# Optimization experiments

Hardware: AMD Instinct MI355X
Metric: run time of the kernel (lower is better)

The kernel has to match this reference:

```python
import jax, jax.numpy as jnp
import numpy as np

B, S, H, V = 32, 400, 512, 50000


def setup_inputs() -> dict:
    key = jax.random.key(0)
    ks = jax.random.split(key, 32)
    g = lambda i, shape: jax.random.normal(ks[i], shape, jnp.float32) * 0.05
    return {
        "x_id": jax.random.randint(ks[0], (B, S), 0, V, jnp.int32),
        "y_id": jax.random.randint(ks[1], (B, 1), 0, V, jnp.int32),
        "x_mask": jnp.zeros((B, S), jnp.int32),  # pad flag: 1 = pad
        "emb": g(2, (V, H)),
        "enc_fw_W": g(3, (H, 3 * H)), "enc_fw_U": g(4, (H, 3 * H)), "enc_fw_b": g(5, (2, 3 * H)),
        "enc_bw_W": g(6, (H, 3 * H)), "enc_bw_U": g(7, (H, 3 * H)), "enc_bw_b": g(8, (2, 3 * H)),
        "red_W": g(9, (2 * H, H)), "red_b": g(10, (H,)),
        "dec_W": g(11, (H, 3 * H)), "dec_U": g(12, (H, 3 * H)), "dec_b": g(13, (2, 3 * H)),
        "att_Wh": g(14, (2 * H, H)), "att_Ws": g(15, (H, H)), "att_bs": g(16, (H,)),
        "att_Wc": g(17, (1, 1)), "att_V": g(18, (H, 1)),
        "fc_W": g(19, (3 * H, H)), "fc_b": g(20, (H,)),
        "vocab_W": g(21, (H, V)),
        "pg_Wh": g(22, (2 * H, 1)), "pg_Ws": g(23, (H, 1)), "pg_Wx": g(24, (H, 1)), "pg_b": g(25, (1,)),
    }


def _gru_cell(h, xz, U, br):
    # Keras GRU, reset_after=True, gate order z, r, h
    hd = h.shape[-1]
    rec = h @ U + br
    z = jax.nn.sigmoid(xz[..., :hd] + rec[..., :hd])
    r = jax.nn.sigmoid(xz[..., hd:2 * hd] + rec[..., hd:2 * hd])
    hh = jnp.tanh(xz[..., 2 * hd:] + r * rec[..., 2 * hd:])
    return z * h + (1.0 - z) * hh


def _gru_scan(x, h0, W, U, b):
    xz = x @ W + b[0]  # [b,T,3H] -- input projections precomputed
    def step(h, xt):
        h = _gru_cell(h, xt, U, b[1])
        return h, h
    h_last, hs = jax.lax.scan(step, h0, jnp.swapaxes(xz, 0, 1))
    return jnp.swapaxes(hs, 0, 1), h_last


def reference(x_id, y_id, x_mask, emb, enc_fw_W, enc_fw_U, enc_fw_b, enc_bw_W, enc_bw_U, enc_bw_b,
              red_W, red_b, dec_W, dec_U, dec_b, att_Wh, att_Ws, att_bs, att_Wc, att_V,
              fc_W, fc_b, vocab_W, pg_Wh, pg_Ws, pg_Wx, pg_b):
    b, s = x_id.shape
    hid = enc_fw_U.shape[0]
    maskf = x_mask.astype(jnp.float32)
    # ---- encoder: single-layer BiGRU ----
    x_emb = emb[x_id]                                     # [b,S,H]
    h0 = jnp.zeros((b, hid), x_emb.dtype)
    fw_seq, fw_s = _gru_scan(x_emb, h0, enc_fw_W, enc_fw_U, enc_fw_b)
    bw_seq, bw_s = _gru_scan(x_emb[:, ::-1], h0, enc_bw_W, enc_bw_U, enc_bw_b)
    enc_seq = jnp.concatenate([fw_seq, bw_seq[:, ::-1]], -1)   # [b,S,2H]
    state = jax.nn.relu(jnp.concatenate([fw_s, bw_s], -1) @ red_W + red_b)  # [b,H]
    # ---- decoder: one GRU step ----
    y_emb = emb[y_id]                                     # [b,1,H]
    xz = y_emb[:, 0] @ dec_W + dec_b[0]
    dec_state = _gru_cell(state, xz, dec_U, dec_b[1])     # [b,H]
    dec_out = dec_state[:, None, :]                       # [b,1,H]
    # ---- Bahdanau attention with (zero-initialized) coverage ----
    e = enc_seq @ att_Wh + (dec_out @ att_Ws + att_bs)    # [b,S,H]
    cover = jnp.zeros((b, s, 1), e.dtype)
    e = e + cover @ att_Wc
    e = jnp.tanh(e) @ att_V                               # [b,S,1]
    e = e + maskf[..., None] * -1e10
    w = jax.nn.softmax(e, axis=-2)                        # [b,S,1]
    context = jnp.sum(w * enc_seq, axis=-2, keepdims=True)  # [b,1,2H]
    # ---- output projection + vocab softmax ----
    y_out = jnp.concatenate([dec_out, context], -1) @ fc_W + fc_b  # [b,1,H]
    vocab_dist = jax.nn.softmax(y_out[:, 0] @ vocab_W, axis=-1)    # [b,V]
    # ---- pointer gate ----
    p_gen = jax.nn.sigmoid(context[:, 0] @ pg_Wh + dec_state @ pg_Ws + y_emb[:, 0] @ pg_Wx + pg_b)  # [b,1]
    # ---- extended-vocab copy distribution (vectorized batched scatter-add) ----
    aw = w[..., 0] * (1.0 - maskf) * (1.0 - p_gen)        # [b,S]
    ext = jnp.pad(p_gen * vocab_dist, ((0, 0), (0, s)))   # [b,V+S]
    bidx = jnp.arange(b)[:, None]
    final = ext.at[bidx, x_id].add(aw)                    # [b,V+S]
    return final
```

## Files before the change

### kernel.cpp

```cpp
#include <hip/hip_runtime.h>
#include <math.h>

#define S_LEN 400
#define BATCH 32
#define HID   512
#define G3    1536
#define N2    3072
#define VOC   50000
#define OUTW  (VOC + S_LEN)

typedef unsigned long long ull;
typedef unsigned int uint;
typedef unsigned short ushort;
typedef short bf16x8 __attribute__((ext_vector_type(8)));
typedef float f32x4 __attribute__((ext_vector_type(4)));
typedef ushort u16x8 __attribute__((ext_vector_type(8)));

__device__ __forceinline__ float sigf(float x) { return 1.f / (1.f + __expf(-x)); }
__device__ __forceinline__ float tanh_fast(float x) {
  const float xc = fminf(fmaxf(x, -15.f), 15.f);
  const float e = __expf(-2.f * xc);
  return (1.f - e) / (1.f + e);
}
__device__ __forceinline__ ushort f2bf(float f) {
  uint u = __float_as_uint(f);
  u += 0x7FFFu + ((u >> 16) & 1u);
  return (ushort)(u >> 16);
}
__device__ __forceinline__ float bf2f(ushort h) {
  return __uint_as_float((uint)h << 16);
}
__device__ __forceinline__ float dot4(float4 a, float4 b) {
  return a.x*b.x + a.y*b.y + a.z*b.z + a.w*b.w;
}

__global__ __launch_bounds__(512) void gru_scan(
    const ushort* __restrict__ xzm,
    const ushort* __restrict__ Utbf,
    const float* __restrict__ bfw, const float* __restrict__ bbw,
    float* __restrict__ enc_seq, ushort* __restrict__ enc_bf,
    ull* __restrict__ hpkt)
{
  const int bid = blockIdx.x;
  const int group = bid & 7;
  const int dir = group >> 2;
  const int bg  = group & 3;
  const int ht  = bid >> 3;
  const int tid = threadIdx.x;
  const int lane = tid & 63;
  const int w  = tid >> 6;
  const int l15 = lane & 15;
  const int lk  = lane >> 4;

  const float* __restrict__ br = (dir ? bbw : bfw) + G3;

  const int gate = w % 3, jh = w / 3;
  bf16x8 ufrag[16];
  if (w < 6) {
    const ushort* ub = Utbf + ((size_t)dir * G3 + gate * 512 + ht * 32 + jh * 16 + l15) * 512
                     + lk * 8;
    #pragma unroll
    for (int s = 0; s < 16; ++s)
      ufrag[s] = *(const bf16x8*)(ub + s * 32);
  }

  __shared__ ushort h_bf[16][520];
  __shared__ float redm[3][8][32];

  for (int i = tid; i < 16 * 520; i += 512) ((ushort*)h_bf)[i] = 0;

  const int cb = w;
  const int gbi = tid >> 5;
  const int gj  = tid & 31;
  const int gjq = ht * 32 + gj;
  const int gb  = bg * 8 + (gbi & 7);
  const float brz = br[gjq], brr = br[512 + gjq], brh = br[1024 + gjq];

  ull* __restrict__ pk = hpkt + (size_t)dir * (2 * BATCH * HID);
  __syncthreads();

  for (int t = 0; t < S_LEN; ++t) {
    const int ts = dir ? (S_LEN - 1 - t) : t;

    float xzv0 = 0.f, xzv1 = 0.f, xzv2 = 0.f;
    if (tid < 256) {
      const ushort* xp = xzm + ((size_t)gb * S_LEN + ts) * N2 + dir * G3 + gjq;
      xzv0 = bf2f(xp[0]); xzv1 = bf2f(xp[512]); xzv2 = bf2f(xp[1024]);
    }

    float hold = 0.f;
    {
      ull* bp = pk + ((size_t)(t & 1) * BATCH + (bg * 8 + cb)) * HID + lane;
      ull* hp = pk + ((size_t)(t & 1) * BATCH + gb) * HID + gjq;
      const uint tu = (uint)t;
      for (;;) {
        ull v0 = __hip_atomic_load(bp,       __ATOMIC_RELAXED, __HIP_MEMORY_SCOPE_AGENT);
        ull v1 = __hip_atomic_load(bp + 64,  __ATOMIC_RELAXED, __HIP_MEMORY_SCOPE_AGENT);
        ull v2 = __hip_atomic_load(bp + 128, __ATOMIC_RELAXED, __HIP_MEMORY_SCOPE_AGENT);
        ull v3 = __hip_atomic_load(bp + 192, __ATOMIC_RELAXED, __HIP_MEMORY_SCOPE_AGENT);
        ull v4 = __hip_atomic_load(bp + 256, __ATOMIC_RELAXED, __HIP_MEMORY_SCOPE_AGENT);
        ull v5 = __hip_atomic_load(bp + 320, __ATOMIC_RELAXED, __HIP_MEMORY_SCOPE_AGENT);
        ull v6 = __hip_atomic_load(bp + 384, __ATOMIC_RELAXED, __HIP_MEMORY_SCOPE_AGENT);
        ull v7 = __hip_atomic_load(bp + 448, __ATOMIC_RELAXED, __HIP_MEMORY_SCOPE_AGENT);
        bool ok = ((uint)(v0 >> 32) == tu) & ((uint)(v1 >> 32) == tu)
                & ((uint)(v2 >> 32) == tu) & ((uint)(v3 >> 32) == tu)
                & ((uint)(v4 >> 32) == tu) & ((uint)(v5 >> 32) == tu)
                & ((uint)(v6 >> 32) == tu) & ((uint)(v7 >> 32) == tu);
        ull hv = 0;
        if (tid < 256) {
          hv = __hip_atomic_load(hp, __ATOMIC_RELAXED, __HIP_MEMORY_SCOPE_AGENT);
          ok &= ((uint)(hv >> 32) == tu);
        }
        if (__all(ok)) {
          h_bf[cb][lane]       = f2bf(__uint_as_float((uint)v0));
          h_bf[cb][lane + 64]  = f2bf(__uint_as_float((uint)v1));
          h_bf[cb][lane + 128] = f2bf(__uint_as_float((uint)v2));
          h_bf[cb][lane + 192] = f2bf(__uint_as_float((uint)v3));
          h_bf[cb][lane + 256] = f2bf(__uint_as_float((uint)v4));
          h_bf[cb][lane + 320] = f2bf(__uint_as_float((uint)v5));
          h_bf[cb][lane + 384] = f2bf(__uint_as_float((uint)v6));
          h_bf[cb][lane + 448] = f2bf(__uint_as_float((uint)v7));
          if (tid < 256) hold = __uint_as_float((uint)hv);
          break;
        }
        __builtin_amdgcn_s_sleep(1);
      }
    }
    __syncthreads();

    if (w < 6) {
      f32x4 acc = f32x4{0.f, 0.f, 0.f, 0.f};
      #pragma unroll
      for (int s = 0; s < 16; ++s) {
        const bf16x8 af = *(const bf16x8*)&h_bf[l15][s * 32 + lk * 8];
        acc = __builtin_amdgcn_mfma_f32_16x16x32_bf16(af, ufrag[s], acc, 0, 0, 0);
      }
      if (lk < 2) {
        #pragma unroll
        for (int r = 0; r < 4; ++r)
          redm[gate][lk * 4 + r][jh * 16 + l15] = acc[r];
      }
    }
    __syncthreads();

    if (tid < 256) {
      const float rz = redm[0][gbi][gj] + brz;
      const float rr = redm[1][gbi][gj] + brr;
      const float rh = redm[2][gbi][gj] + brh;
      const float z  = sigf(xzv0 + rz);
      const float r  = sigf(xzv1 + rr);
      const float hh = tanh_fast(xzv2 + r * rh);
      const float hnew = z * hold + (1.f - z) * hh;
      const ull pack = ((ull)(uint)(t + 1) << 32) | (ull)__float_as_uint(hnew);
      __hip_atomic_store(pk + ((size_t)((t + 1) & 1) * BATCH + gb) * HID + gjq,
                         pack, __ATOMIC_RELAXED, __HIP_MEMORY_SCOPE_AGENT);
      const size_t eidx = ((size_t)gb * S_LEN + ts) * 1024 + dir * 512 + gjq;
      enc_seq[eidx] = hnew;
      enc_bf[eidx]  = f2bf(hnew);
    }
    __syncthreads();
  }
}

__global__ __launch_bounds__(256) void k_transW(
    const float* __restrict__ srcA, const float* __restrict__ srcB,
    const int split, const int srcStride, const int Krows,
    ushort* __restrict__ dst,
    const float* __restrict__ biasA, const float* __restrict__ biasB,
    float* __restrict__ bm)
{
  __shared__ float t[64][65];
  const int k0 = blockIdx.x * 64, n0 = blockIdx.y * 64;
  const int tid = threadIdx.x;
  const int j = tid & 63, i0 = tid >> 6;
  {
    const int n = n0 + j;
    const float* s = (n < split) ? (srcA + n) : (srcB + (n - split));
    #pragma unroll
    for (int i = i0; i < 64; i += 4)
      t[i][j] = s[(size_t)(k0 + i) * srcStride];
  }
  __syncthreads();
  const int ii = tid & 63;
  #pragma unroll
  for (int jj = i0; jj < 64; jj += 4)
    dst[(size_t)(n0 + jj) * Krows + k0 + ii] = f2bf(t[ii][jj]);
  if (bm != nullptr && k0 == 0 && tid < 64) {
    const int n = n0 + tid;
    bm[n] = (n < split) ? biasA[n] : biasB[n - split];
  }
}

__global__ __launch_bounds__(256) void k_transF(
    const float* __restrict__ srcA, const float* __restrict__ srcB,
    const int split, const int srcStride, const int Krows,
    float* __restrict__ dst)
{
  __shared__ float t[64][65];
  const int k0 = blockIdx.x * 64, n0 = blockIdx.y * 64;
  const int tid = threadIdx.x;
  const int j = tid & 63, i0 = tid >> 6;
  {
    const int n = n0 + j;
    const float* s = (n < split) ? (srcA + n) : (srcB + (n - split));
    #pragma unroll
    for (int i = i0; i < 64; i += 4)
      t[i][j] = s[(size_t)(k0 + i) * srcStride];
  }
  __syncthreads();
  const int ii = tid & 63;
  #pragma unroll
  for (int jj = i0; jj < 64; jj += 4)
    dst[(size_t)(n0 + jj) * Krows + k0 + ii] = t[ii][jj];
}

__global__ __launch_bounds__(256) void gemm_bf16(
    const int* __restrict__ x_id, const float* __restrict__ emb,
    const ushort* __restrict__ Bt,
    const float* __restrict__ bias,
    ushort* __restrict__ C)
{
  const int m0 = blockIdx.y * 128, n0 = blockIdx.x * 128;
  const int tid = threadIdx.x;
  const int w = tid >> 6, lane = tid & 63;
  const int l15 = lane & 15, lk = lane >> 4;
  __shared__ short As[128][40];
  __shared__ short Bs[128][40];
  __shared__ int rid[128];
  if (tid < 128) rid[tid] = x_id[m0 + tid];
  f32x4 acc[2][8];
  #pragma unroll
  for (int i = 0; i < 2; ++i)
    #pragma unroll
    for (int j = 0; j < 8; ++j) acc[i][j] = f32x4{0.f, 0.f, 0.f, 0.f};

  const int sr = tid >> 1;
  const int sc = (tid & 1) * 8;
  __syncthreads();
  const float* arow = emb + (size_t)rid[sr] * 512;

  for (int k0 = 0; k0 < 512; k0 += 32) {
    const float4 f0 = *(const float4*)(arow + k0 + sc);
    const float4 f1 = *(const float4*)(arow + k0 + sc + 4);
    const float4 f2 = *(const float4*)(arow + k0 + 16 + sc);
    const float4 f3 = *(const float4*)(arow + k0 + 16 + sc + 4);
    const uint4 b0 = *(const uint4*)&Bt[(size_t)(n0 + sr) * 512 + k0 + sc];
    const uint4 b1 = *(const uint4*)&Bt[(size_t)(n0 + sr) * 512 + k0 + 16 + sc];
    u16x8 a0, a1;
    a0[0]=f2bf(f0.x); a0[1]=f2bf(f0.y); a0[2]=f2bf(f0.z); a0[3]=f2bf(f0.w);
    a0[4]=f2bf(f1.x); a0[5]=f2bf(f1.y); a0[6]=f2bf(f1.z); a0[7]=f2bf(f1.w);
    a1[0]=f2bf(f2.x); a1[1]=f2bf(f2.y); a1[2]=f2bf(f2.z); a1[3]=f2bf(f2.w);
    a1[4]=f2bf(f3.x); a1[5]=f2bf(f3.y); a1[6]=f2bf(f3.z); a1[7]=f2bf(f3.w);
    *(u16x8*)&As[sr][sc]      = a0;
    *(u16x8*)&As[sr][16 + sc] = a1;
    *(uint4*)&Bs[sr][sc]      = b0;
    *(uint4*)&Bs[sr][16 + sc] = b1;
    __syncthreads();

    bf16x8 af[2], bfr[8];
    #pragma unroll
    for (int rf = 0; rf < 2; ++rf)
      af[rf] = *(const bf16x8*)&As[w * 32 + rf * 16 + l15][lk * 8];
    #pragma unroll
    for (int cf = 0; cf < 8; ++cf)
      bfr[cf] = *(const bf16x8*)&Bs[cf * 16 + l15][lk * 8];
    #pragma unroll
    for (int rf = 0; rf < 2; ++rf)
      #pragma unroll
      for (int cf = 0; cf < 8; ++cf)
        acc[rf][cf] = __builtin_amdgcn_mfma_f32_16x16x32_bf16(
            af[rf], bfr[cf], acc[rf][cf], 0, 0, 0);
    __syncthreads();
  }

  #pragma unroll
  for (int rf = 0; rf < 2; ++rf) {
    #pragma unroll
    for (int cf = 0; cf < 8; ++cf) {
      const int col = n0 + cf * 16 + l15;
      const float bv = bias[col];
      const int rowb = m0 + w * 32 + rf * 16 + lk * 4;
      #pragma unroll
      for (int r = 0; r < 4; ++r)
        C[(size_t)(rowb + r) * N2 + col] = f2bf(acc[rf][cf][r] + bv);
    }
  }
}

__global__ __launch_bounds__(256) void gemm_att(
    const ushort* __restrict__ A,
    const ushort* __restrict__ Bt,
    const float* __restrict__ dterm,
    const float* __restrict__ attV,
    float* __restrict__ e_part)
{
  const int m0 = blockIdx.y * 128, n0 = blockIdx.x * 128;
  const int tid = threadIdx.x;
  const int w = tid >> 6, lane = tid & 63;
  const int l15 = lane & 15, lk = lane >> 4;
  __shared__ short As[128][40];
  __shared__ short Bs[128][40];
  f32x4 acc[2][8];
  #pragma unroll
  for (int i = 0; i < 2; ++i)
    #pragma unroll
    for (int j = 0; j < 8; ++j) acc[i][j] = f32x4{0.f, 0.f, 0.f, 0.f};

  const int sr = tid >> 1;
  const int sc = (tid & 1) * 8;

  for (int k0 = 0; k0 < 1024; k0 += 32) {
    const uint4 a0 = *(const uint4*)&A[(size_t)(m0 + sr) * 1024 + k0 + sc];
    const uint4 a1 = *(const uint4*)&A[(size_t)(m0 + sr) * 1024 + k0 + 16 + sc];
    const uint4 b0 = *(const uint4*)&Bt[(size_t)(n0 + sr) * 1024 + k0 + sc];
    const uint4 b1 = *(const uint4*)&Bt[(size_t)(n0 + sr) * 1024 + k0 + 16 + sc];
    *(uint4*)&As[sr][sc]      = a0;
    *(uint4*)&As[sr][16 + sc] = a1;
    *(uint4*)&Bs[sr][sc]      = b0;
    *(uint4*)&Bs[sr][16 + sc] = b1;
    __syncthreads();

    bf16x8 af[2], bfr[8];
    #pragma unroll
    for (int rf = 0; rf < 2; ++rf)
      af[rf] = *(const bf16x8*)&As[w * 32 + rf * 16 + l15][lk * 8];
    #pragma unroll
    for (int cf = 0; cf < 8; ++cf)
      bfr[cf] = *(const bf16x8*)&Bs[cf * 16 + l15][lk * 8];
    #pragma unroll
    for (int rf = 0; rf < 2; ++rf)
      #pragma unroll
      for (int cf = 0; cf < 8; ++cf)
        acc[rf][cf] = __builtin_amdgcn_mfma_f32_16x16x32_bf16(
            af[rf], bfr[cf], acc[rf][cf], 0, 0, 0);
    __syncthreads();
  }

  #pragma unroll
  for (int rf = 0; rf < 2; ++rf) {
    #pragma unroll
    for (int r = 0; r < 4; ++r) {
      const int row = m0 + w * 32 + rf * 16 + lk * 4 + r;
      const int b = row / S_LEN;
      float p = 0.f;
      #pragma unroll
      for (int cf = 0; cf < 8; ++cf) {
        const int col = n0 + cf * 16 + l15;
        p += attV[col] * tanh_fast(acc[rf][cf][r] + dterm[(size_t)b * 512 + col]);
      }
      p += __shfl_xor(p, 1); p += __shfl_xor(p, 2);
      p += __shfl_xor(p, 4); p += __shfl_xor(p, 8);
      if (l15 == 0) e_part[(size_t)row * 4 + blockIdx.x] = p;
    }
  }
}

__global__ __launch_bounds__(128) void k_state(const float* __restrict__ enc,
    const float* __restrict__ redWt,
    const float* __restrict__ red_b, float* __restrict__ state)
{
  const int b = blockIdx.y;
  const int j = blockIdx.x*128 + threadIdx.x;
  const float4* wr = (const float4*)(redWt + (size_t)j * 1024);
  const float4* fw = (const float4*)(enc + ((size_t)b*S_LEN + (S_LEN-1))*1024);
  const float4* bw = (const float4*)(enc + ((size_t)b*S_LEN)*1024 + 512);
  float acc = red_b[j];
  #pragma unroll 4
  for (int k = 0; k < 128; ++k) acc += dot4(fw[k], wr[k]);
  #pragma unroll 4
  for (int k = 0; k < 128; ++k) acc += dot4(bw[k], wr[128 + k]);
  state[(size_t)b*512 + j] = fmaxf(acc, 0.f);
}

__global__ __launch_bounds__(128) void k_dec(
    const int* __restrict__ y_id, const float* __restrict__ emb,
    const float* __restrict__ state,
    const float* __restrict__ decWUt,
    const float* __restrict__ dec_b, float* __restrict__ dst)
{
  const int b = blockIdx.y;
  const int j = blockIdx.x*128 + threadIdx.x;
  const float4* ye = (const float4*)(emb + (size_t)y_id[b] * 512);
  const float4* st = (const float4*)(state + (size_t)b * 512);
  const float4* w0 = (const float4*)(decWUt + (size_t)(j)        * 512);
  const float4* w1 = (const float4*)(decWUt + (size_t)(512  + j) * 512);
  const float4* w2 = (const float4*)(decWUt + (size_t)(1024 + j) * 512);
  const float4* u0 = (const float4*)(decWUt + (size_t)(G3 + j)        * 512);
  const float4* u1 = (const float4*)(decWUt + (size_t)(G3 + 512  + j) * 512);
  const float4* u2 = (const float4*)(decWUt + (size_t)(G3 + 1024 + j) * 512);
  float xz0 = dec_b[j], xz1 = dec_b[512+j], xz2 = dec_b[1024+j];
  float rc0 = dec_b[G3+j], rc1 = dec_b[G3+512+j], rc2 = dec_b[G3+1024+j];
  #pragma unroll 2
  for (int k = 0; k < 128; ++k) {
    const float4 yv = ye[k], sv = st[k];
    xz0 += dot4(yv, w0[k]); xz1 += dot4(yv, w1[k]); xz2 += dot4(yv, w2[k]);
    rc0 += dot4(sv, u0[k]); rc1 += dot4(sv, u1[k]); rc2 += dot4(sv, u2[k]);
  }
  const float z  = sigf(xz0 + rc0);
  const float r  = sigf(xz1 + rc1);
  const float hh = tanh_fast(xz2 + r*rc2);
  const float sj = state[(size_t)b*512 + j];
  dst[(size_t)b*512 + j] = z*sj + (1.f-z)*hh;
}

__global__ __launch_bounds__(128) void k_dterm(const float* __restrict__ dec,
    const float* __restrict__ WsT,
    const float* __restrict__ att_bs, float* __restrict__ dterm)
{
  const int b = blockIdx.y;
  const int j = blockIdx.x*128 + threadIdx.x;
  const float4* d = (const float4*)(dec + (size_t)b*512);
  const float4* wr = (const float4*)(WsT + (size_t)j * 512);
  float acc = att_bs[j];
  #pragma unroll 4
  for (int k = 0; k < 128; ++k) acc += dot4(d[k], wr[k]);
  dterm[(size_t)b*512 + j] = acc;
}

__global__ __launch_bounds__(512) void k_soft(const float* __restrict__ e_part,
    const int* __restrict__ x_mask, float* __restrict__ wat)
{
  const int b = blockIdx.x, tid = threadIdx.x;
  __shared__ float sm[512];
  float e = -1e30f, ev = 0.f;
  if (tid < S_LEN) {
    const float* ep = e_part + (size_t)(b*S_LEN + tid)*4;
    ev = ep[0]+ep[1]+ep[2]+ep[3] + (float)x_mask[b*S_LEN+tid] * -1e10f;
    e = ev;
  }
  sm[tid] = e; __syncthreads();
  for (int s = 256; s > 0; s >>= 1) { if (tid < s) sm[tid] = fmaxf(sm[tid], sm[tid+s]); __syncthreads(); }
  const float m = sm[0]; __syncthreads();
  const float x = (tid < S_LEN) ? __expf(ev - m) : 0.f;
  sm[tid] = x; __syncthreads();
  for (int s = 256; s > 0; s >>= 1) { if (tid < s) sm[tid] += sm[tid+s]; __syncthreads(); }
  const float inv = 1.f / sm[0];
  if (tid < S_LEN) wat[b*S_LEN+tid] = x * inv;
}

__global__ __launch_bounds__(128) void k_ctx(const float* __restrict__ wat,
    const float* __restrict__ enc, float* __restrict__ ctx)
{
  const int b = blockIdx.y;
  const int j = blockIdx.x*128 + threadIdx.x;
  float acc = 0.f;
  const float* w = wat + b*S_LEN;
  const float* ep = enc + (size_t)b*S_LEN*1024 + j;
  #pragma unroll 4
  for (int s = 0; s < S_LEN; ++s) acc += w[s] * ep[(size_t)s*1024];
  ctx[(size_t)b*1024 + j] = acc;
}

__global__ __launch_bounds__(128) void k_yout(const float* __restrict__ dec,
    const float* __restrict__ ctx,
    const float* __restrict__ fcT,
    const float* __restrict__ fc_b, float* __restrict__ y_out)
{
  const int b = blockIdx.y;
  const int j = blockIdx.x*128 + threadIdx.x;
  const float4* d = (const float4*)(dec + (size_t)b*512);
  const float4* c = (const float4*)(ctx + (size_t)b*1024);
  const float4* wr = (const float4*)(fcT + (size_t)j * 1536);
  float acc = fc_b[j];
  #pragma unroll 4
  for (int k = 0; k < 128; ++k) acc += dot4(d[k], wr[k]);
  #pragma unroll 4
  for (int k = 0; k < 256; ++k) acc += dot4(c[k], wr[128 + k]);
  y_out[(size_t)b*512 + j] = acc;
}

__global__ __launch_bounds__(256) void k_pgen(const float* __restrict__ ctx,
    const float* __restrict__ dec,
    const int* __restrict__ y_id, const float* __restrict__ emb,
    const float* __restrict__ pg_Wh, const float* __restrict__ pg_Ws,
    const float* __restrict__ pg_Wx, const float* __restrict__ pg_b,
    float* __restrict__ pg)
{
  const int b = blockIdx.x, tid = threadIdx.x;
  __shared__ float sm[256];
  const float* ye = emb + (size_t)y_id[b] * 512;
  float acc = 0.f;
  for (int k = tid; k < 1024; k += 256) acc += ctx[(size_t)b*1024+k]*pg_Wh[k];
  for (int k = tid; k < 512;  k += 256) acc += dec[(size_t)b*512+k]*pg_Ws[k] + ye[k]*pg_Wx[k];
  sm[tid] = acc; __syncthreads();
  for (int s = 128; s > 0; s >>= 1) { if (tid < s) sm[tid] += sm[tid+s]; __syncthreads(); }
  if (tid == 0) pg[b] = sigf(sm[0] + pg_b[0]);
}

__global__ __launch_bounds__(256) void k_vocab(const float* __restrict__ y_out,
    const float* __restrict__ vocab_W, float* __restrict__ logits)
{
  __shared__ float y_lds[256][32];
  const int tid = threadIdx.x;
  const int vq = tid & 63, bq = tid >> 6;
  const int v = blockIdx.x * 256 + vq * 4;
  float acc[8][4];
  #pragma unroll
  for (int i = 0; i < 8; ++i)
    #pragma unroll
    for (int j = 0; j < 4; ++j) acc[i][j] = 0.f;
  for (int half = 0; half < 2; ++half) {
    __syncthreads();
    for (int i = 0; i < 32; ++i) {
      const int idx = tid + 256*i;
      const int k = idx >> 5, b = idx & 31;
      y_lds[k][b] = y_out[(size_t)b*512 + half*256 + k];
    }
    __syncthreads();
    if (v < VOC) {
      #pragma unroll 4
      for (int k = 0; k < 256; ++k) {
        const float4 wv = *(const float4*)&vocab_W[(size_t)(half*256 + k) * VOC + v];
        const float4 ya = *(const float4*)&y_lds[k][bq*8];
        const float4 yb = *(const float4*)&y_lds[k][bq*8+4];
        const float yy[8] = {ya.x,ya.y,ya.z,ya.w,yb.x,yb.y,yb.z,yb.w};
        #pragma unroll
        for (int i = 0; i < 8; ++i) {
          acc[i][0] += yy[i]*wv.x; acc[i][1] += yy[i]*wv.y;
          acc[i][2] += yy[i]*wv.z; acc[i][3] += yy[i]*wv.w;
        }
      }
    }
  }
  if (v < VOC) {
    #pragma unroll
    for (int i = 0; i < 8; ++i)
      *(float4*)&logits[(size_t)(bq*8+i)*VOC + v] = make_float4(acc[i][0],acc[i][1],acc[i][2],acc[i][3]);
  }
}

__global__ __launch_bounds__(1024) void k_vred(const float* __restrict__ logits,
                                               float* __restrict__ red2)
{
  const int b = blockIdx.x, tid = threadIdx.x;
  __shared__ float sm[1024];
  float m = -1e30f;
  for (int i = tid; i < VOC; i += 1024) m = fmaxf(m, logits[(size_t)b*VOC + i]);
  sm[tid] = m; __syncthreads();
  for (int s = 512; s > 0; s >>= 1) { if (tid < s) sm[tid] = fmaxf(sm[tid], sm[tid+s]); __syncthreads(); }
  m = sm[0]; __syncthreads();
  float sum = 0.f;
  for (int i = tid; i < VOC; i += 1024) sum += __expf(logits[(size_t)b*VOC + i] - m);
  sm[tid] = sum; __syncthreads();
  for (int s = 512; s > 0; s >>= 1) { if (tid < s) sm[tid] += sm[tid+s]; __syncthreads(); }
  if (tid == 0) { red2[b*2] = m; red2[b*2+1] = sm[0]; }
}

__global__ __launch_bounds__(256) void k_final(const float* __restrict__ logits,
    const float* __restrict__ red2, const float* __restrict__ pg,
    float* __restrict__ out)
{
  const size_t idx = (size_t)blockIdx.x*256 + threadIdx.x;
  const int b = (int)(idx / OUTW);
  const int c = (int)(idx - (size_t)b*OUTW);
  float v = 0.f;
  if (c < VOC) {
    const float m = red2[b*2], s = red2[b*2+1];
    v = pg[b] * __expf(logits[(size_t)b*VOC + c] - m) / s;
  }
  out[idx] = v;
}

__global__ __launch_bounds__(256) void k_scatter(const float* __restrict__ wat,
    const int* __restrict__ x_mask, const float* __restrict__ pg,
    const int* __restrict__ x_id, float* __restrict__ out)
{
  const int i = blockIdx.x*256 + threadIdx.x;
  const int b = i / S_LEN;
  const float aw = wat[i] * (1.f - (float)x_mask[i]) * (1.f - pg[b]);
  atomicAdd(out + (size_t)b*OUTW + x_id[i], aw);
}

extern "C" void kernel_launch(void* const* d_in, const int* in_sizes, int n_in,
                              void* d_out, int out_size, void* d_ws, size_t ws_size,
                              hipStream_t stream)
{
  (void)in_sizes; (void)n_in; (void)out_size; (void)ws_size;
  const int*   x_id     = (const int*)d_in[0];
  const int*   y_id     = (const int*)d_in[1];
  const int*   x_mask   = (const int*)d_in[2];
  const float* emb      = (const float*)d_in[3];
  const float* enc_fw_W = (const float*)d_in[4];
  const float* enc_fw_U = (const float*)d_in[5];
  const float* enc_fw_b = (const float*)d_in[6];
  const float* enc_bw_W = (const float*)d_in[7];
  const float* enc_bw_U = (const float*)d_in[8];
  const float* enc_bw_b = (const float*)d_in[9];
  const float* red_W    = (const float*)d_in[10];
  const float* red_b    = (const float*)d_in[11];
  const float* dec_W    = (const float*)d_in[12];
  const float* dec_U    = (const float*)d_in[13];
  const float* dec_b    = (const float*)d_in[14];
  const float* att_Wh   = (const float*)d_in[15];
  const float* att_Ws   = (const float*)d_in[16];
  const float* att_bs   = (const float*)d_in[17];
  const float* att_Wc   = (const float*)d_in[18]; (void)att_Wc;
  const float* att_V    = (const float*)d_in[19];
  const float* fc_W     = (const float*)d_in[20];
  const float* fc_b     = (const float*)d_in[21];
  const float* vocab_W  = (const float*)d_in[22];
  const float* pg_Wh    = (const float*)d_in[23];
  const float* pg_Ws    = (const float*)d_in[24];
  const float* pg_Wx    = (const float*)d_in[25];
  const float* pg_b     = (const float*)d_in[26];
  float* out = (float*)d_out;

  const size_t NPKT = (size_t)2*2*BATCH*HID;
  char* p = (char*)d_ws;
  ushort* xzm   = (ushort*)p; p += (size_t)BATCH*S_LEN*N2*2;
  float*  enc   = (float*)p;  p += (size_t)BATCH*S_LEN*1024*4;
  ushort* encbf = (ushort*)p; p += (size_t)BATCH*S_LEN*1024*2;
  ull*   hpkt   = (ull*)p;    p += NPKT*8;
  ushort* Wt    = (ushort*)p; p += (size_t)N2*512*2;
  ushort* Whbf  = (ushort*)p; p += (size_t)512*1024*2;
  ushort* Utbf  = (ushort*)p; p += (size_t)2*G3*512*2;
  float*  redWt = (float*)p;  p += (size_t)512*1024*4;
  float*  decWUt= (float*)p;  p += (size_t)N2*512*4;
  float*  WsT   = (float*)p;  p += (size_t)512*512*4;
  float*  fcT   = (float*)p;  p += (size_t)512*1536*4;
  float*  bm    = (float*)p;  p += (size_t)N2*4;
  float*  fstate = (float*)p; p += (size_t)BATCH*HID*4;
  float*  decs   = (float*)p; p += (size_t)BATCH*HID*4;
  float*  dterm  = (float*)p; p += (size_t)BATCH*HID*4;
  float*  epart  = (float*)p; p += (size_t)BATCH*S_LEN*4*4;
  float*  wat    = (float*)p; p += (size_t)BATCH*S_LEN*4;
  float*  ctx    = (float*)p; p += (size_t)BATCH*1024*4;
  float*  yout   = (float*)p; p += (size_t)BATCH*HID*4;
  float*  pg     = (float*)p; p += (size_t)256*4;
  float*  logits = (float*)p; p += (size_t)BATCH*VOC*4;
  float*  red2   = (float*)p; p += (size_t)64*4;

  hipMemsetAsync(hpkt, 0, NPKT * sizeof(ull), stream);

  k_transW<<<dim3(512/64, N2/64), 256, 0, stream>>>(
      enc_fw_W, enc_bw_W, G3, G3, 512, Wt, enc_fw_b, enc_bw_b, bm);
  k_transW<<<dim3(1024/64, 512/64), 256, 0, stream>>>(
      att_Wh, att_Wh, 512, 512, 1024, Whbf, nullptr, nullptr, nullptr);
  k_transW<<<dim3(512/64, G3/64), 256, 0, stream>>>(
      enc_fw_U, enc_fw_U, G3, G3, 512, Utbf, nullptr, nullptr, nullptr);
  k_transW<<<dim3(512/64, G3/64), 256, 0, stream>>>(
      enc_bw_U, enc_bw_U, G3, G3, 512, Utbf + (size_t)G3*512, nullptr, nullptr, nullptr);
  k_transF<<<dim3(1024/64, 512/64), 256, 0, stream>>>(
      red_W, red_W, 512, 512, 1024, redWt);
  k_transF<<<dim3(512/64, N2/64), 256, 0, stream>>>(
      dec_W, dec_U, G3, G3, 512, decWUt);
  k_transF<<<dim3(512/64, 512/64), 256, 0, stream>>>(
      att_Ws, att_Ws, 512, 512, 512, WsT);
  k_transF<<<dim3(1536/64, 512/64), 256, 0, stream>>>(
      fc_W, fc_W, 512, 512, 1536, fcT);
  gemm_bf16<<<dim3(N2/128, BATCH*S_LEN/128), 256, 0, stream>>>(x_id, emb, Wt, bm, xzm);
  gru_scan<<<128,512,0,stream>>>(xzm, Utbf, enc_fw_b, enc_bw_b,
                                 enc, encbf, hpkt);
  k_state<<<dim3(4,32),128,0,stream>>>(enc, redWt, red_b, fstate);
  k_dec<<<dim3(4,32),128,0,stream>>>(y_id, emb, fstate, decWUt, dec_b, decs);
  k_dterm<<<dim3(4,32),128,0,stream>>>(decs, WsT, att_bs, dterm);
  gemm_att<<<dim3(4, BATCH*S_LEN/128), 256, 0, stream>>>(encbf, Whbf, dterm,
                                                         att_V, epart);
  k_soft<<<32,512,0,stream>>>(epart, x_mask, wat);
  k_ctx<<<dim3(8,32),128,0,stream>>>(wat, enc, ctx);
  k_yout<<<dim3(4,32),128,0,stream>>>(decs, ctx, fcT, fc_b, yout);
  k_pgen<<<32,256,0,stream>>>(ctx, decs, y_id, emb, pg_Wh, pg_Ws, pg_Wx, pg_b, pg);
  k_vocab<<<196,256,0,stream>>>(yout, vocab_W, logits);
  k_vred<<<32,1024,0,stream>>>(logits, red2);
  k_final<<<6300,256,0,stream>>>(logits, red2, pg, out);
  k_scatter<<<50,256,0,stream>>>(wat, x_mask, pg, x_id, out);
}
```

Baseline: 1.397 ms.

## Overlap weight transposes with GRU scan and pre-convert embeddings to bf16

Transposes that are only needed after the encoder (attention, reduce, decoder, fc weights) now run as extra blocks appended to the gru_scan launch, so they execute on idle CUs while the latency-bound recurrence runs. The remaining encoder transposes are merged into one kernel launch. A new k_cvtA kernel gathers the embeddings and converts them to bf16 once, so gemm_bf16 loads bf16 A tiles directly instead of converting fp32 inside its inner loop. This cuts launch count and per-tile conversion work, but adds an extra write and read of the bf16 activation buffer. The extra blocks could also compete with the scan's persistent blocks for scheduling and memory bandwidth.

```diff
diff --git a/kernel.cpp b/kernel.cpp
--- a/kernel.cpp
+++ b/kernel.cpp
@@ -34,13 +34,73 @@
   return a.x*b.x + a.y*b.y + a.z*b.z + a.w*b.w;
 }
 
+__device__ void trans_tile_512(const float* __restrict__ srcA,
+                               const float* __restrict__ srcB,
+                               const int split, const int stride, const int Krows,
+                               const int k0, const int n0,
+                               ushort* __restrict__ dstH, float* __restrict__ dstF)
+{
+  __shared__ float tt[64][65];
+  const int tid = threadIdx.x;
+  const int j = tid & 63, i0 = tid >> 6;
+  {
+    const int n = n0 + j;
+    const float* s = (n < split) ? (srcA + n) : (srcB + (n - split));
+    #pragma unroll
+    for (int i = i0; i < 64; i += 8)
+      tt[i][j] = s[(size_t)(k0 + i) * stride];
+  }
+  __syncthreads();
+  const int ii = tid & 63;
+  if (dstH != nullptr) {
+    #pragma unroll
+    for (int jj = i0; jj < 64; jj += 8)
+      dstH[(size_t)(n0 + jj) * Krows + k0 + ii] = f2bf(tt[ii][jj]);
+  } else {
+    #pragma unroll
+    for (int jj = i0; jj < 64; jj += 8)
+      dstF[(size_t)(n0 + jj) * Krows + k0 + ii] = tt[ii][jj];
+  }
+}
+
 __global__ __launch_bounds__(512) void gru_scan(
     const ushort* __restrict__ xzm,
     const ushort* __restrict__ Utbf,
     const float* __restrict__ bfw, const float* __restrict__ bbw,
     float* __restrict__ enc_seq, ushort* __restrict__ enc_bf,
-    ull* __restrict__ hpkt)
-{
+    ull* __restrict__ hpkt,
+    const float* __restrict__ att_Wh, const float* __restrict__ red_W,
+    const float* __restrict__ dec_W, const float* __restrict__ dec_U,
+    const float* __restrict__ att_Ws, const float* __restrict__ fc_W,
+    ushort* __restrict__ Whbf, float* __restrict__ redWt,
+    float* __restrict__ decWUt, float* __restrict__ WsT,
+    float* __restrict__ fcT)
+{
+  if (blockIdx.x >= 128) {
+    const int tb = blockIdx.x - 128;
+    if (tb < 128) {
+      trans_tile_512(att_Wh, att_Wh, 512, 512, 1024,
+                     (tb % 16) * 64, (tb / 16) * 64, Whbf, nullptr);
+    } else if (tb < 256) {
+      const int t = tb - 128;
+      trans_tile_512(red_W, red_W, 512, 512, 1024,
+                     (t % 16) * 64, (t / 16) * 64, nullptr, redWt);
+    } else if (tb < 640) {
+      const int t = tb - 256;
+      trans_tile_512(dec_W, dec_U, G3, G3, 512,
+                     (t % 8) * 64, (t / 8) * 64, nullptr, decWUt);
+    } else if (tb < 704) {
+      const int t = tb - 640;
+      trans_tile_512(att_Ws, att_Ws, 512, 512, 512,
+                     (t % 8) * 64, (t / 8) * 64, nullptr, WsT);
+    } else {
+      const int t = tb - 704;
+      trans_tile_512(fc_W, fc_W, 512, 512, 1536,
+                     (t % 24) * 64, (t / 24) * 64, nullptr, fcT);
+    }
+    return;
+  }
+
   const int bid = blockIdx.x;
   const int group = bid & 7;
   const int dir = group >> 2;
@@ -162,60 +222,61 @@
   }
 }
 
-__global__ __launch_bounds__(256) void k_transW(
-    const float* __restrict__ srcA, const float* __restrict__ srcB,
-    const int split, const int srcStride, const int Krows,
-    ushort* __restrict__ dst,
-    const float* __restrict__ biasA, const float* __restrict__ biasB,
-    float* __restrict__ bm)
-{
-  __shared__ float t[64][65];
-  const int k0 = blockIdx.x * 64, n0 = blockIdx.y * 64;
+__global__ __launch_bounds__(256) void k_cvtA(
+    const int* __restrict__ x_id, const float* __restrict__ emb,
+    ushort* __restrict__ Abf)
+{
+  const int tid = threadIdx.x;
+  const int row = blockIdx.x * 4 + (tid >> 6);
+  const int k8 = (tid & 63) * 8;
+  const int rid = x_id[row];
+  const float4 e0 = *(const float4*)&emb[(size_t)rid * 512 + k8];
+  const float4 e1 = *(const float4*)&emb[(size_t)rid * 512 + k8 + 4];
+  u16x8 o;
+  o[0] = f2bf(e0.x); o[1] = f2bf(e0.y); o[2] = f2bf(e0.z); o[3] = f2bf(e0.w);
+  o[4] = f2bf(e1.x); o[5] = f2bf(e1.y); o[6] = f2bf(e1.z); o[7] = f2bf(e1.w);
+  *(u16x8*)&Abf[(size_t)row * 512 + k8] = o;
+}
+
+__global__ __launch_bounds__(256) void k_transUp(
+    const float* __restrict__ fwW, const float* __restrict__ bwW,
+    const float* __restrict__ fwb, const float* __restrict__ bwb,
+    const float* __restrict__ fwU, const float* __restrict__ bwU,
+    ushort* __restrict__ Wt, float* __restrict__ bm,
+    ushort* __restrict__ Utbf)
+{
+  __shared__ float tt[64][65];
+  const int b = blockIdx.x;
   const int tid = threadIdx.x;
   const int j = tid & 63, i0 = tid >> 6;
+  const float* srcA; const float* srcB; int split, k0, n0; ushort* dst;
+  if (b < 384)      { srcA = fwW; srcB = bwW; split = G3;
+                      k0 = (b % 8) * 64; n0 = (b / 8) * 64; dst = Wt; }
+  else if (b < 576) { const int t = b - 384; srcA = fwU; srcB = fwU; split = N2;
+                      k0 = (t % 8) * 64; n0 = (t / 8) * 64; dst = Utbf; }
+  else              { const int t = b - 576; srcA = bwU; srcB = bwU; split = N2;
+                      k0 = (t % 8) * 64; n0 = (t / 8) * 64;
+                      dst = Utbf + (size_t)G3 * 512; }
   {
     const int n = n0 + j;
     const float* s = (n < split) ? (srcA + n) : (srcB + (n - split));
     #pragma unroll
     for (int i = i0; i < 64; i += 4)
-      t[i][j] = s[(size_t)(k0 + i) * srcStride];
+      tt[i][j] = s[(size_t)(k0 + i) * G3];
   }
   __syncthreads();
   const int ii = tid & 63;
   #pragma unroll
   for (int jj = i0; jj < 64; jj += 4)
-    dst[(size_t)(n0 + jj) * Krows + k0 + ii] = f2bf(t[ii][jj]);
-  if (bm != nullptr && k0 == 0 && tid < 64) {
+    dst[(size_t)(n0 + jj) * 512 + k0 + ii] = f2bf(tt[ii][jj]);
+  if (b < 384 && k0 == 0 && tid < 64) {
     const int n = n0 + tid;
-    bm[n] = (n < split) ? biasA[n] : biasB[n - split];
-  }
-}
-
-__global__ __launch_bounds__(256) void k_transF(
-    const float* __restrict__ srcA, const float* __restrict__ srcB,
-    const int split, const int srcStride, const int Krows,
-    float* __restrict__ dst)
-{
-  __shared__ float t[64][65];
-  const int k0 = blockIdx.x * 64, n0 = blockIdx.y * 64;
-  const int tid = threadIdx.x;
-  const int j = tid & 63, i0 = tid >> 6;
-  {
-    const int n = n0 + j;
-    const float* s = (n < split) ? (srcA + n) : (srcB + (n - split));
-    #pragma unroll
-    for (int i = i0; i < 64; i += 4)
-      t[i][j] = s[(size_t)(k0 + i) * srcStride];
-  }
-  __syncthreads();
-  const int ii = tid & 63;
-  #pragma unroll
-  for (int jj = i0; jj < 64; jj += 4)
-    dst[(size_t)(n0 + jj) * Krows + k0 + ii] = t[ii][jj];
+    bm[n] = (n < G3) ? fwb[n] : bwb[n - G3];
+  }
 }
 
 __global__ __launch_bounds__(256) void gemm_bf16(
-    const int* __restrict__ x_id, const float* __restrict__ emb,
+    const ushort* __restrict__ A,
     const ushort* __restrict__ Bt,
     const float* __restrict__ bias,
     ushort* __restrict__ C)
@@ -226,8 +287,6 @@
   const int l15 = lane & 15, lk = lane >> 4;
   __shared__ short As[128][40];
   __shared__ short Bs[128][40];
-  __shared__ int rid[128];
-  if (tid < 128) rid[tid] = x_id[m0 + tid];
   f32x4 acc[2][8];
   #pragma unroll
   for (int i = 0; i < 2; ++i)
@@ -236,23 +295,14 @@
 
   const int sr = tid >> 1;
   const int sc = (tid & 1) * 8;
-  __syncthreads();
-  const float* arow = emb + (size_t)rid[sr] * 512;
 
   for (int k0 = 0; k0 < 512; k0 += 32) {
-    const float4 f0 = *(const float4*)(arow + k0 + sc);
-    const float4 f1 = *(const float4*)(arow + k0 + sc + 4);
-    const float4 f2 = *(const float4*)(arow + k0 + 16 + sc);
-    const float4 f3 = *(const float4*)(arow + k0 + 16 + sc + 4);
+    const uint4 a0 = *(const uint4*)&A[(size_t)(m0 + sr) * 512 + k0 + sc];
+    const uint4 a1 = *(const uint4*)&A[(size_t)(m0 + sr) * 512 + k0 + 16 + sc];
     const uint4 b0 = *(const uint4*)&Bt[(size_t)(n0 + sr) * 512 + k0 + sc];
     const uint4 b1 = *(const uint4*)&Bt[(size_t)(n0 + sr) * 512 + k0 + 16 + sc];
-    u16x8 a0, a1;
-    a0[0]=f2bf(f0.x); a0[1]=f2bf(f0.y); a0[2]=f2bf(f0.z); a0[3]=f2bf(f0.w);
-    a0[4]=f2bf(f1.x); a0[5]=f2bf(f1.y); a0[6]=f2bf(f1.z); a0[7]=f2bf(f1.w);
-    a1[0]=f2bf(f2.x); a1[1]=f2bf(f2.y); a1[2]=f2bf(f2.z); a1[3]=f2bf(f2.w);
-    a1[4]=f2bf(f3.x); a1[5]=f2bf(f3.y); a1[6]=f2bf(f3.z); a1[7]=f2bf(f3.w);
-    *(u16x8*)&As[sr][sc]      = a0;
-    *(u16x8*)&As[sr][16 + sc] = a1;
+    *(uint4*)&As[sr][sc]      = a0;
+    *(uint4*)&As[sr][16 + sc] = a1;
     *(uint4*)&Bs[sr][sc]      = b0;
     *(uint4*)&Bs[sr][16 + sc] = b1;
     __syncthreads();
@@ -611,6 +661,7 @@
   float*  enc   = (float*)p;  p += (size_t)BATCH*S_LEN*1024*4;
   ushort* encbf = (ushort*)p; p += (size_t)BATCH*S_LEN*1024*2;
   ull*   hpkt   = (ull*)p;    p += NPKT*8;
+  ushort* Abf   = (ushort*)p; p += (size_t)BATCH*S_LEN*512*2;
   ushort* Wt    = (ushort*)p; p += (size_t)N2*512*2;
   ushort* Whbf  = (ushort*)p; p += (size_t)512*1024*2;
   ushort* Utbf  = (ushort*)p; p += (size_t)2*G3*512*2;
@@ -632,25 +683,14 @@
 
   hipMemsetAsync(hpkt, 0, NPKT * sizeof(ull), stream);
 
-  k_transW<<<dim3(512/64, N2/64), 256, 0, stream>>>(
-      enc_fw_W, enc_bw_W, G3, G3, 512, Wt, enc_fw_b, enc_bw_b, bm);
-  k_transW<<<dim3(1024/64, 512/64), 256, 0, stream>>>(
-      att_Wh, att_Wh, 512, 512, 1024, Whbf, nullptr, nullptr, nullptr);
-  k_transW<<<dim3(512/64, G3/64), 256, 0, stream>>>(
-      enc_fw_U, enc_fw_U, G3, G3, 512, Utbf, nullptr, nullptr, nullptr);
-  k_transW<<<dim3(512/64, G3/64), 256, 0, stream>>>(
-      enc_bw_U, enc_bw_U, G3, G3, 512, Utbf + (size_t)G3*512, nullptr, nullptr, nullptr);
-  k_transF<<<dim3(1024/64, 512/64), 256, 0, stream>>>(
-      red_W, red_W, 512, 512, 1024, redWt);
-  k_transF<<<dim3(512/64, N2/64), 256, 0, stream>>>(
-      dec_W, dec_U, G3, G3, 512, decWUt);
-  k_transF<<<dim3(512/64, 512/64), 256, 0, stream>>>(
-      att_Ws, att_Ws, 512, 512, 512, WsT);
-  k_transF<<<dim3(1536/64, 512/64), 256, 0, stream>>>(
-      fc_W, fc_W, 512, 512, 1536, fcT);
-  gemm_bf16<<<dim3(N2/128, BATCH*S_LEN/128), 256, 0, stream>>>(x_id, emb, Wt, bm, xzm);
-  gru_scan<<<128,512,0,stream>>>(xzm, Utbf, enc_fw_b, enc_bw_b,
-                                 enc, encbf, hpkt);
+  k_cvtA<<<BATCH*S_LEN/4, 256, 0, stream>>>(x_id, emb, Abf);
+  k_transUp<<<768, 256, 0, stream>>>(enc_fw_W, enc_bw_W, enc_fw_b, enc_bw_b,
+                                     enc_fw_U, enc_bw_U, Wt, bm, Utbf);
+  gemm_bf16<<<dim3(N2/128, BATCH*S_LEN/128), 256, 0, stream>>>(Abf, Wt, bm, xzm);
+  gru_scan<<<128 + 896, 512, 0, stream>>>(xzm, Utbf, enc_fw_b, enc_bw_b,
+                                          enc, encbf, hpkt,
+                                          att_Wh, red_W, dec_W, dec_U, att_Ws,
+                                          fc_W, Whbf, redWt, decWUt, WsT, fcT);
   k_state<<<dim3(4,32),128,0,stream>>>(enc, redWt, red_b, fstate);
   k_dec<<<dim3(4,32),128,0,stream>>>(y_id, emb, fstate, decWUt, dec_b, decs);
   k_dterm<<<dim3(4,32),128,0,stream>>>(decs, WsT, att_bs, dterm);
```

After: 1.326 ms. -5.1%, faster.
